# Optimization experiments

Measured on AMD Instinct MI355X. Metric: run time of the kernel, lower is better.

The kernel has to match this reference:

```python
import jax, jax.numpy as jnp
import numpy as np

Q_NODES = 100000
S_NODES = 100000
N_EDGES = 3200000
D = 3
HIDDEN = 64
OUT_DIM = 128
STAT_DIM = 3 + 2 * D  # N_i, D_avg, D_var, Delta(D), PCA(D)


def setup_inputs() -> dict:
    key = jax.random.key(0)
    ks = jax.random.split(key, 7)
    source_pos = jax.random.normal(ks[0], (S_NODES, D), dtype=jnp.float32)
    query_pos = jax.random.normal(ks[1], (Q_NODES, D), dtype=jnp.float32)
    qi = jax.random.randint(ks[2], (N_EDGES,), 0, Q_NODES, dtype=jnp.int64)
    si = jax.random.randint(ks[3], (N_EDGES,), 0, S_NODES, dtype=jnp.int64)
    edge_index = jnp.stack([qi, si], axis=0)
    # MLP params (torch Linear default-ish scale)
    W1 = jax.random.normal(ks[4], (HIDDEN, STAT_DIM), dtype=jnp.float32) / np.sqrt(STAT_DIM)
    b1 = jnp.zeros((HIDDEN,), dtype=jnp.float32)
    W2 = jax.random.normal(ks[5], (OUT_DIM, HIDDEN), dtype=jnp.float32) / np.sqrt(HIDDEN)
    b2 = jnp.zeros((OUT_DIM,), dtype=jnp.float32)
    return {"source_pos": source_pos, "query_pos": query_pos, "edge_index": edge_index,
            "W1": W1, "b1": b1, "W2": W2, "b2": b2}


def _stat_features(source_pos, query_pos, edge_index):
    Q = query_pos.shape[0]
    qi = edge_index[0]
    si = edge_index[1]
    ones = jnp.ones(qi.shape, dtype=jnp.float32)
    counts = jax.ops.segment_sum(ones, qi, num_segments=Q)          # [Q] = N_i
    has = counts > 0
    Nc = jnp.where(has, counts, 1.0)                                 # clamp 0 -> 1

    nbr = source_pos[si]                                             # [E,D]
    qc = query_pos[qi]                                               # [E,D]
    dist = jnp.linalg.norm(nbr - qc, axis=1)                         # [E]
    D_avg = jax.ops.segment_sum(dist, qi, num_segments=Q) / Nc       # [Q]
    E_X2 = jax.ops.segment_sum(dist * dist, qi, num_segments=Q) / Nc
    D_var = jnp.maximum(E_X2 - D_avg * D_avg, 0.0)

    centroid = jax.ops.segment_sum(nbr, qi, num_segments=Q) / Nc[:, None]  # [Q,D]
    Delta = centroid - query_pos                                     # [Q,D]

    centered = nbr - centroid[qi]                                    # [E,D]
    cov_comp = centered[:, :, None] * centered[:, None, :]           # [E,D,D]
    cov = jax.ops.segment_sum(cov_comp, qi, num_segments=Q) / Nc[:, None, None]

    eig = jnp.linalg.eigvalsh(cov)[:, ::-1]                          # descending [Q,D]
    PCA = jnp.where(has[:, None], eig, 0.0)

    feats = jnp.concatenate([counts[:, None], D_avg[:, None], D_var[:, None], Delta, PCA], axis=1)
    feats = jnp.where(has[:, None], feats, 0.0)

    mean = feats.mean(axis=0, keepdims=True)
    std = jnp.std(feats, axis=0, ddof=1, keepdims=True)              # torch std is unbiased
    std = jnp.where(std < 1e-6, 1.0, std)
    return (feats - mean) / std


def reference(source_pos, query_pos, edge_index, W1, b1, W2, b2):
    feats = _stat_features(source_pos, query_pos, edge_index)        # [Q, 9]
    h = jax.nn.relu(feats @ W1.T + b1)
    return h @ W2.T + b2                                             # [Q, OUT_DIM]
```

## Files before the change

kernel.cpp:

```cpp
#include <hip/hip_runtime.h>
#include <math.h>

#define Q_NODES 100000
#define S_NODES 100000
#define N_EDGES 3200000
#define HIDDEN 64
#define OUT_DIM 128

#define QPB   128
#define NB    782
#define CAPB  4608
#define TILE  8192
#define NT4   (N_EDGES / 4)

#define F_CURSOR_OFF 0
#define F_NORM_OFF   3200
#define F_PSUM_OFF   3328
#define F_PSUMSQ_OFF 31488
#define F_FEATS_OFF  59648
#define F_SP4_OFF    3659648
#define F_SLOTS_OFF  5259648
#define F_ZERO_BYTES 3200
#define F_WS_NEED    (5259648ull + (unsigned long long)(NB * CAPB + 1) * 4)

#define B_ACC_OFF    0
#define B_STATS_OFF  4800000
#define B_NORM_OFF   4800144
#define B_FEATS_OFF  4800224
#define B_ZERO_BYTES 4800144

__device__ __forceinline__ void atomAddF(float* p, float v) {
#if defined(__gfx950__) || defined(__gfx942__) || defined(__gfx90a__)
    unsafeAtomicAdd(p, v);
#else
    atomicAdd(p, v);
#endif
}


__device__ __forceinline__ void eig3_sym(
        float a00, float a01, float a02, float a11, float a12, float a22,
        float& e1, float& e2, float& e3) {
    float p1 = a01 * a01 + a02 * a02 + a12 * a12;
    float qm = (a00 + a11 + a22) * (1.0f / 3.0f);
    float b00 = a00 - qm, b11 = a11 - qm, b22 = a22 - qm;
    float p2 = b00 * b00 + b11 * b11 + b22 * b22 + 2.0f * p1;
    if (p2 <= 1e-24f) {
        e1 = qm; e2 = qm; e3 = qm;
    } else {
        float p = sqrtf(p2 * (1.0f / 6.0f));
        float invp = 1.0f / p;
        float c00 = b00 * invp, c11 = b11 * invp, c22 = b22 * invp;
        float c01 = a01 * invp, c02 = a02 * invp, c12 = a12 * invp;
        float detB = c00 * (c11 * c22 - c12 * c12)
                   - c01 * (c01 * c22 - c12 * c02)
                   + c02 * (c01 * c12 - c11 * c02);
        float r = 0.5f * detB;
        r = fminf(fmaxf(r, -1.0f), 1.0f);
        float phi = acosf(r) * (1.0f / 3.0f);
        e1 = qm + 2.0f * p * cosf(phi);
        e3 = qm + 2.0f * p * cosf(phi + 2.0943951023931953f);
        e2 = 3.0f * qm - e1 - e3;
    }
}

__device__ __forceinline__ void sums_to_feats(
        const float* s, float qx, float qy, float qz, float* f) {
    float n = s[0];
#pragma unroll
    for (int k = 0; k < 9; ++k) f[k] = 0.0f;
    if (n > 0.0f) {
        float inv = 1.0f / n;
        float Davg = s[1] * inv;
        float Dvar = fmaxf(s[2] * inv - Davg * Davg, 0.0f);
        float cx = s[3] * inv, cy = s[4] * inv, cz = s[5] * inv;
        float a00 = fmaxf(s[6] * inv - cx * cx, 0.0f);
        float a01 = s[7] * inv - cx * cy;
        float a02 = s[8] * inv - cx * cz;
        float a11 = fmaxf(s[9] * inv - cy * cy, 0.0f);
        float a12 = s[10] * inv - cy * cz;
        float a22 = fmaxf(s[11] * inv - cz * cz, 0.0f);
        float e1, e2, e3;
        eig3_sym(a00, a01, a02, a11, a12, a22, e1, e2, e3);
        f[0] = n; f[1] = Davg; f[2] = Dvar;
        f[3] = cx - qx; f[4] = cy - qy; f[5] = cz - qz;
        f[6] = e1; f[7] = e2; f[8] = e3;
    }
}


__global__ __launch_bounds__(512, 4) void partition_kernel(
        const int* __restrict__ edge,
        const float* __restrict__ sp,
        float4* __restrict__ sp4,
        int* __restrict__ cursor,
        unsigned int* __restrict__ slots) {
    __shared__ unsigned int s_rec[TILE];
    __shared__ int s_posh[TILE];
    __shared__ int s_cur[NB];
    __shared__ int s_off[NB];
    __shared__ int s_wsum[8];

    int tid = threadIdx.x;
    int lane = tid & 63, wv = tid >> 6;
    int tileStart = blockIdx.x * TILE;
    int tileCount = N_EDGES - tileStart;
    if (tileCount > TILE) tileCount = TILE;

    {
        int i = blockIdx.x * 512 + tid;
        if (i < S_NODES)
            sp4[i] = make_float4(sp[3 * i], sp[3 * i + 1], sp[3 * i + 2], 0.0f);
    }

    for (int b = tid; b < NB; b += 512) s_posh[b] = 0;
    __syncthreads();

    const int4* eq4 = (const int4*)edge;
    const int4* es4 = (const int4*)(edge + N_EDGES);
    int base4 = blockIdx.x * (TILE / 4);
    int4 q4[4], s4[4];
    bool v[4];
#pragma unroll
    for (int j = 0; j < 4; ++j) {
        int i4 = base4 + tid + j * 512;
        v[j] = i4 < NT4;
        int ic = v[j] ? i4 : 0;
        q4[j] = eq4[ic];
        s4[j] = es4[ic];
        if (v[j]) {
            atomicAdd(&s_posh[q4[j].x >> 7], 1);
            atomicAdd(&s_posh[q4[j].y >> 7], 1);
            atomicAdd(&s_posh[q4[j].z >> 7], 1);
            atomicAdd(&s_posh[q4[j].w >> 7], 1);
        }
    }
    __syncthreads();

    int local[2], tsum = 0;
#pragma unroll
    for (int j = 0; j < 2; ++j) {
        int idx = 2 * tid + j;
        local[j] = (idx < NB) ? s_posh[idx] : 0;
        tsum += local[j];
    }
    int inc = tsum;
#pragma unroll
    for (int off = 1; off < 64; off <<= 1) {
        int t = __shfl_up(inc, off);
        if (lane >= off) inc += t;
    }
    if (lane == 63) s_wsum[wv] = inc;
    __syncthreads();
    int wbase = 0;
    for (int w = 0; w < wv; ++w) wbase += s_wsum[w];
    int run = wbase + inc - tsum;
#pragma unroll
    for (int j = 0; j < 2; ++j) {
        int idx = 2 * tid + j;
        if (idx < NB) s_cur[idx] = run;
        run += local[j];
    }
    __syncthreads();

    for (int b = tid; b < NB; b += 512) {
        int c = s_posh[b];
        int base = c ? atomicAdd(&cursor[b], c) : 0;
        s_off[b] = b * CAPB + base - s_cur[b];
    }
    __syncthreads();

#pragma unroll
    for (int j = 0; j < 4; ++j) {
        if (v[j]) {
            int qs[4] = { q4[j].x, q4[j].y, q4[j].z, q4[j].w };
            int ss[4] = { s4[j].x, s4[j].y, s4[j].z, s4[j].w };
#pragma unroll
            for (int m = 0; m < 4; ++m) {
                int bkt = qs[m] >> 7;
                int idx = atomicAdd(&s_cur[bkt], 1);
                int gpos = idx + s_off[bkt];
                if (gpos >= (bkt + 1) * CAPB) gpos = NB * CAPB;
                s_rec[idx] = ((unsigned)(qs[m] & (QPB - 1)) << 17) | (unsigned)ss[m];
                s_posh[idx] = gpos;
            }
        }
    }
    __syncthreads();

    for (int i = tid; i < tileCount; i += 512)
        slots[s_posh[i]] = s_rec[i];
}

__global__ __launch_bounds__(512) void bucket_kernel(
        const int* __restrict__ cursor,
        const unsigned int* __restrict__ slots,
        const float4* __restrict__ sp4,
        const float* __restrict__ qp,
        float* __restrict__ feats,
        float* __restrict__ psum,
        float* __restrict__ psumsq) {
    __shared__ unsigned int s_sorted[CAPB];
    __shared__ float qtile[QPB * 3];
    __shared__ int s_cnt[QPB], s_start[QPB], s_cur[QPB];
    __shared__ float s_part[4][QPB][13];
    __shared__ float s_red1[8][9], s_red2[8][9];

    int tid = threadIdx.x;
    int b = blockIdx.x;
    int cnt = cursor[b];
    if (cnt > CAPB) cnt = CAPB;

    if (tid < QPB) s_cnt[tid] = 0;
    for (int i = tid; i < QPB * 3; i += 512) {
        int g = b * QPB * 3 + i;
        qtile[i] = (g < Q_NODES * 3) ? qp[g] : 0.0f;
    }
    __syncthreads();

    const unsigned int* bslots = slots + b * CAPB;
    for (int i = tid; i < cnt; i += 512)
        atomicAdd(&s_cnt[bslots[i] >> 17], 1);
    __syncthreads();

    if (tid < 64) {
        int a0 = s_cnt[tid], a1 = s_cnt[64 + tid];
        int i0 = a0, i1 = a1;
#pragma unroll
        for (int off = 1; off < 64; off <<= 1) {
            int t0 = __shfl_up(i0, off); if (tid >= off) i0 += t0;
            int t1 = __shfl_up(i1, off); if (tid >= off) i1 += t1;
        }
        int tot0 = __shfl(i0, 63);
        s_start[tid] = i0 - a0;              s_cur[tid] = i0 - a0;
        s_start[64 + tid] = i1 - a1 + tot0;  s_cur[64 + tid] = i1 - a1 + tot0;
    }
    __syncthreads();

    for (int i = tid; i < cnt; i += 512) {
        unsigned rec = bslots[i];
        int pos = atomicAdd(&s_cur[rec >> 17], 1);
        s_sorted[pos] = rec;
    }
    __syncthreads();

    {
        int q = tid & (QPB - 1);
        int sub = tid >> 7;
        float qx = qtile[3 * q + 0], qy = qtile[3 * q + 1], qz = qtile[3 * q + 2];
        float s[12];
#pragma unroll
        for (int k = 0; k < 12; ++k) s[k] = 0.0f;
        int st = s_start[q], deg = s_cnt[q];
        for (int j = sub; j < deg; j += 4) {
            unsigned rec = s_sorted[st + j];
            float4 sv = sp4[rec & 0x1FFFF];
            float dx = sv.x - qx, dy = sv.y - qy, dz = sv.z - qz;
            float d2 = dx * dx + dy * dy + dz * dz;
            s[0] += 1.0f;
            s[1] += sqrtf(d2);
            s[2] += d2;
            s[3] += sv.x; s[4] += sv.y; s[5] += sv.z;
            s[6] += sv.x * sv.x; s[7] += sv.x * sv.y; s[8] += sv.x * sv.z;
            s[9] += sv.y * sv.y; s[10] += sv.y * sv.z; s[11] += sv.z * sv.z;
        }
#pragma unroll
        for (int k = 0; k < 12; ++k) s_part[sub][q][k] = s[k];
    }
    __syncthreads();

    float f[9];
#pragma unroll
    for (int k = 0; k < 9; ++k) f[k] = 0.0f;
    int q = b * QPB + (tid & (QPB - 1));
    if (tid < QPB && q < Q_NODES) {
        float qx = qtile[3 * tid + 0], qy = qtile[3 * tid + 1], qz = qtile[3 * tid + 2];
        float s[12];
#pragma unroll
        for (int k = 0; k < 12; ++k)
            s[k] = ((s_part[0][tid][k] + s_part[1][tid][k])
                  + (s_part[2][tid][k] + s_part[3][tid][k]));
        sums_to_feats(s, qx, qy, qz, f);
#pragma unroll
        for (int k = 0; k < 9; ++k) feats[k * Q_NODES + q] = f[k];
    }

    int lane = tid & 63, wv = tid >> 6;
#pragma unroll
    for (int k = 0; k < 9; ++k) {
        float s1 = f[k];
        float s2 = f[k] * f[k];
#pragma unroll
        for (int off = 32; off > 0; off >>= 1) {
            s1 += __shfl_down(s1, off);
            s2 += __shfl_down(s2, off);
        }
        if (lane == 0) { s_red1[wv][k] = s1; s_red2[wv][k] = s2; }
    }
    __syncthreads();
    if (tid < 9) {
        float t1 = 0.0f, t2 = 0.0f;
#pragma unroll
        for (int w = 0; w < 8; ++w) { t1 += s_red1[w][tid]; t2 += s_red2[w][tid]; }
        psum[tid * NB + b]   = t1;
        psumsq[tid * NB + b] = t2;
    }
}

__global__ __launch_bounds__(576) void stats_reduce_kernel(
        const float* __restrict__ psum,
        const float* __restrict__ psumsq,
        float* __restrict__ norm) {
    int k = threadIdx.x >> 6, lane = threadIdx.x & 63;
    if (k >= 9) return;
    double a1 = 0.0, a2 = 0.0;
    for (int b = lane; b < NB; b += 64) {
        a1 += (double)psum[k * NB + b];
        a2 += (double)psumsq[k * NB + b];
    }
#pragma unroll
    for (int off = 32; off > 0; off >>= 1) {
        a1 += __shfl_down(a1, off);
        a2 += __shfl_down(a2, off);
    }
    if (lane == 0) {
        double S = a1, S2 = a2;
        double mean = S / (double)Q_NODES;
        double var = (S2 - S * S / (double)Q_NODES) / (double)(Q_NODES - 1);
        if (var < 0.0) var = 0.0;
        double sd = sqrt(var);
        if (sd < 1e-6) sd = 1.0;
        norm[k] = (float)mean;
        norm[9 + k] = (float)(1.0 / sd);
    }
}


__global__ __launch_bounds__(512, 6) void mlp_kernel(
        const float* __restrict__ feats,
        const float* __restrict__ norm,
        const float* __restrict__ W1, const float* __restrict__ b1,
        const float* __restrict__ W2, const float* __restrict__ b2,
        float* __restrict__ out) {
    __shared__ float sW1[576];
    __shared__ float sB1[64];
    __shared__ float sB2[128];
    __shared__ float sNorm[18];
    __shared__ float w2t[64 * 64];
    __shared__ float ht[64 * 128];

    int tid = threadIdx.x;
    int blk_q = blockIdx.x;

    for (int i = tid; i < 576; i += 512) sW1[i] = W1[i];
    if (tid < 64) sB1[tid] = b1[tid];
    if (tid < 128) sB2[tid] = b2[tid];
    if (tid < 18) sNorm[tid] = norm[tid];

    {
        int o = tid & 63, kc = (tid >> 6) * 8;
#pragma unroll
        for (int j = 0; j < 8; ++j) {
            int k = kc + j;
            w2t[k * 64 + o] = W2[o * 64 + k];
        }
    }
    __syncthreads();

    {
        int q = tid & 127, quarter = tid >> 7;
        int qg = blk_q * 128 + q;
        int qc = qg < Q_NODES ? qg : Q_NODES - 1;
        float f[9];
#pragma unroll
        for (int k = 0; k < 9; ++k)
            f[k] = (feats[k * Q_NODES + qc] - sNorm[k]) * sNorm[9 + k];
#pragma unroll 4
        for (int j = 0; j < 16; ++j) {
            int ko = quarter * 16 + j;
            float a = sB1[ko];
#pragma unroll
            for (int kf = 0; kf < 9; ++kf) a = fmaf(f[kf], sW1[ko * 9 + kf], a);
            ht[ko * 128 + q] = fmaxf(a, 0.0f);
        }
    }
    __syncthreads();

    int qt = tid >> 4, ot = tid & 15;
    int q0 = qt * 4, o0 = ot * 4;

#pragma unroll 1
    for (int pass = 0; pass < 2; ++pass) {
        int oh = pass * 64;
        if (pass) {
            __syncthreads();
            int o = tid & 63, kc = (tid >> 6) * 8;
#pragma unroll
            for (int j = 0; j < 8; ++j) {
                int k = kc + j;
                w2t[k * 64 + o] = W2[(oh + o) * 64 + k];
            }
            __syncthreads();
        }

        float acc[4][4];
#pragma unroll
        for (int i = 0; i < 4; ++i)
#pragma unroll
            for (int j = 0; j < 4; ++j) acc[i][j] = 0.0f;

#pragma unroll 4
        for (int k = 0; k < 64; ++k) {
            float4 h = *(const float4*)&ht[k * 128 + q0];
            float4 w = *(const float4*)&w2t[k * 64 + o0];
            float hh[4] = { h.x, h.y, h.z, h.w };
#pragma unroll
            for (int i = 0; i < 4; ++i) {
                acc[i][0] = fmaf(hh[i], w.x, acc[i][0]);
                acc[i][1] = fmaf(hh[i], w.y, acc[i][1]);
                acc[i][2] = fmaf(hh[i], w.z, acc[i][2]);
                acc[i][3] = fmaf(hh[i], w.w, acc[i][3]);
            }
        }

        float4 bb = *(const float4*)&sB2[oh + o0];
#pragma unroll
        for (int i = 0; i < 4; ++i) {
            int qg = blk_q * 128 + q0 + i;
            if (qg < Q_NODES) {
                float4 vv = make_float4(acc[i][0] + bb.x, acc[i][1] + bb.y,
                                        acc[i][2] + bb.z, acc[i][3] + bb.w);
                *(float4*)(out + (size_t)qg * 128 + oh + o0) = vv;
            }
        }
    }
}


__global__ __launch_bounds__(256) void edge_kernel(
        const int* __restrict__ edge,
        const float* __restrict__ sp,
        const float* __restrict__ qp,
        float* __restrict__ acc) {
    int e = blockIdx.x * 256 + threadIdx.x;
    if (e >= N_EDGES) return;
    int q = edge[e];
    int s = edge[N_EDGES + e];
    float sx = sp[3 * s + 0], sy = sp[3 * s + 1], sz = sp[3 * s + 2];
    float qx = qp[3 * q + 0], qy = qp[3 * q + 1], qz = qp[3 * q + 2];
    float dx = sx - qx, dy = sy - qy, dz = sz - qz;
    float d2 = dx * dx + dy * dy + dz * dz;
    atomAddF(acc + 0 * Q_NODES + q, 1.0f);
    atomAddF(acc + 1 * Q_NODES + q, sqrtf(d2));
    atomAddF(acc + 2 * Q_NODES + q, d2);
    atomAddF(acc + 3 * Q_NODES + q, sx);
    atomAddF(acc + 4 * Q_NODES + q, sy);
    atomAddF(acc + 5 * Q_NODES + q, sz);
    atomAddF(acc + 6 * Q_NODES + q, sx * sx);
    atomAddF(acc + 7 * Q_NODES + q, sx * sy);
    atomAddF(acc + 8 * Q_NODES + q, sx * sz);
    atomAddF(acc + 9 * Q_NODES + q, sy * sy);
    atomAddF(acc + 10 * Q_NODES + q, sy * sz);
    atomAddF(acc + 11 * Q_NODES + q, sz * sz);
}

__global__ __launch_bounds__(256) void finalize_kernel(
        const float* __restrict__ acc,
        const float* __restrict__ qp,
        float* __restrict__ feats,
        double* __restrict__ stats) {
    int q = blockIdx.x * 256 + threadIdx.x;
    float f[9];
#pragma unroll
    for (int k = 0; k < 9; ++k) f[k] = 0.0f;
    if (q < Q_NODES) {
        float s[12];
#pragma unroll
        for (int k = 0; k < 12; ++k) s[k] = acc[k * Q_NODES + q];
        float qx = qp[3 * q + 0], qy = qp[3 * q + 1], qz = qp[3 * q + 2];
        sums_to_feats(s, qx, qy, qz, f);
#pragma unroll
        for (int k = 0; k < 9; ++k) feats[k * Q_NODES + q] = f[k];
    }
    int lane = threadIdx.x & 63;
#pragma unroll
    for (int k = 0; k < 9; ++k) {
        float s1 = f[k];
        float s2 = f[k] * f[k];
#pragma unroll
        for (int off = 32; off > 0; off >>= 1) {
            s1 += __shfl_down(s1, off);
            s2 += __shfl_down(s2, off);
        }
        if (lane == 0) {
            atomicAdd(&stats[k], (double)s1);
            atomicAdd(&stats[9 + k], (double)s2);
        }
    }
}

__global__ void stats_kernel(const double* __restrict__ stats,
                             float* __restrict__ norm) {
    int k = threadIdx.x;
    if (k < 9) {
        double S = stats[k], S2 = stats[9 + k];
        double mean = S / (double)Q_NODES;
        double var = (S2 - S * S / (double)Q_NODES) / (double)(Q_NODES - 1);
        if (var < 0.0) var = 0.0;
        double sd = sqrt(var);
        if (sd < 1e-6) sd = 1.0;
        norm[k] = (float)mean;
        norm[9 + k] = (float)(1.0 / sd);
    }
}


extern "C" void kernel_launch(void* const* d_in, const int* in_sizes, int n_in,
                              void* d_out, int out_size, void* d_ws, size_t ws_size,
                              hipStream_t stream) {
    const float* sp   = (const float*)d_in[0];
    const float* qp   = (const float*)d_in[1];
    const int*   edge = (const int*)d_in[2];
    const float* W1   = (const float*)d_in[3];
    const float* b1   = (const float*)d_in[4];
    const float* W2   = (const float*)d_in[5];
    const float* b2   = (const float*)d_in[6];
    float* out = (float*)d_out;
    char* ws = (char*)d_ws;

    if (ws_size >= F_WS_NEED) {
        int*          cursor = (int*)(ws + F_CURSOR_OFF);
        float*        norm   = (float*)(ws + F_NORM_OFF);
        float*        psum   = (float*)(ws + F_PSUM_OFF);
        float*        psumsq = (float*)(ws + F_PSUMSQ_OFF);
        float*        feats  = (float*)(ws + F_FEATS_OFF);
        float4*       sp4    = (float4*)(ws + F_SP4_OFF);
        unsigned int* slots  = (unsigned int*)(ws + F_SLOTS_OFF);

        hipMemsetAsync(ws, 0, F_ZERO_BYTES, stream);
        partition_kernel<<<(N_EDGES + TILE - 1) / TILE, 512, 0, stream>>>(
            edge, sp, sp4, cursor, slots);
        bucket_kernel<<<NB, 512, 0, stream>>>(
            cursor, slots, sp4, qp, feats, psum, psumsq);
        stats_reduce_kernel<<<1, 576, 0, stream>>>(psum, psumsq, norm);
        mlp_kernel<<<NB, 512, 0, stream>>>(feats, norm, W1, b1, W2, b2, out);
    } else {
        float*  acc   = (float*)(ws + B_ACC_OFF);
        double* stats = (double*)(ws + B_STATS_OFF);
        float*  norm  = (float*)(ws + B_NORM_OFF);
        float*  feats = (float*)(ws + B_FEATS_OFF);

        hipMemsetAsync(ws, 0, B_ZERO_BYTES, stream);
        edge_kernel<<<N_EDGES / 256, 256, 0, stream>>>(edge, sp, qp, acc);
        finalize_kernel<<<(Q_NODES + 255) / 256, 256, 0, stream>>>(acc, qp, feats, stats);
        stats_kernel<<<1, 64, 0, stream>>>(stats, norm);
        mlp_kernel<<<NB, 512, 0, stream>>>(feats, norm, W1, b1, W2, b2, out);
    }
}
```

Baseline: 184.9 us.

## Restructure MLP second layer to read W2 via wave-uniform scalar loads

```diff
diff --git a/kernel.cpp b/kernel.cpp
--- a/kernel.cpp
+++ b/kernel.cpp
@@ -346,7 +346,6 @@
     __shared__ float sB1[64];
     __shared__ float sB2[128];
     __shared__ float sNorm[18];
-    __shared__ float w2t[64 * 64];
     __shared__ float ht[64 * 128];
 
     int tid = threadIdx.x;
@@ -356,15 +355,6 @@
     if (tid < 64) sB1[tid] = b1[tid];
     if (tid < 128) sB2[tid] = b2[tid];
     if (tid < 18) sNorm[tid] = norm[tid];
-
-    {
-        int o = tid & 63, kc = (tid >> 6) * 8;
-#pragma unroll
-        for (int j = 0; j < 8; ++j) {
-            int k = kc + j;
-            w2t[k * 64 + o] = W2[o * 64 + k];
-        }
-    }
     __syncthreads();
 
     {
@@ -386,52 +376,69 @@
     }
     __syncthreads();
 
-    int qt = tid >> 4, ot = tid & 15;
-    int q0 = qt * 4, o0 = ot * 4;
-
-#pragma unroll 1
-    for (int pass = 0; pass < 2; ++pass) {
-        int oh = pass * 64;
-        if (pass) {
-            __syncthreads();
-            int o = tid & 63, kc = (tid >> 6) * 8;
-#pragma unroll
-            for (int j = 0; j < 8; ++j) {
-                int k = kc + j;
-                w2t[k * 64 + o] = W2[(oh + o) * 64 + k];
-            }
-            __syncthreads();
-        }
-
-        float acc[4][4];
-#pragma unroll
-        for (int i = 0; i < 4; ++i)
-#pragma unroll
-            for (int j = 0; j < 4; ++j) acc[i][j] = 0.0f;
-
-#pragma unroll 4
-        for (int k = 0; k < 64; ++k) {
-            float4 h = *(const float4*)&ht[k * 128 + q0];
-            float4 w = *(const float4*)&w2t[k * 64 + o0];
-            float hh[4] = { h.x, h.y, h.z, h.w };
-#pragma unroll
-            for (int i = 0; i < 4; ++i) {
-                acc[i][0] = fmaf(hh[i], w.x, acc[i][0]);
-                acc[i][1] = fmaf(hh[i], w.y, acc[i][1]);
-                acc[i][2] = fmaf(hh[i], w.z, acc[i][2]);
-                acc[i][3] = fmaf(hh[i], w.w, acc[i][3]);
-            }
-        }
-
-        float4 bb = *(const float4*)&sB2[oh + o0];
-#pragma unroll
-        for (int i = 0; i < 4; ++i) {
-            int qg = blk_q * 128 + q0 + i;
-            if (qg < Q_NODES) {
-                float4 vv = make_float4(acc[i][0] + bb.x, acc[i][1] + bb.y,
-                                        acc[i][2] + bb.z, acc[i][3] + bb.w);
-                *(float4*)(out + (size_t)qg * 128 + oh + o0) = vv;
-            }
+    int lane = tid & 63;
+    int wvu = __builtin_amdgcn_readfirstlane(tid >> 6);
+    int o0 = wvu * 16;
+    const float4* wrow = (const float4*)(W2 + (size_t)o0 * 64);
+
+    float acc0[16], acc1[16];
+#pragma unroll
+    for (int o = 0; o < 16; ++o) { acc0[o] = 0.0f; acc1[o] = 0.0f; }
+
+    for (int kc = 0; kc < 16; ++kc) {
+        float4 w[16];
+#pragma unroll
+        for (int o = 0; o < 16; ++o) w[o] = wrow[o * 16 + kc];
+        int kb = kc * 4;
+        float h0a = ht[(kb + 0) * 128 + lane];
+        float h0b = ht[(kb + 1) * 128 + lane];
+        float h0c = ht[(kb + 2) * 128 + lane];
+        float h0d = ht[(kb + 3) * 128 + lane];
+        float h1a = ht[(kb + 0) * 128 + 64 + lane];
+        float h1b = ht[(kb + 1) * 128 + 64 + lane];
+        float h1c = ht[(kb + 2) * 128 + 64 + lane];
+        float h1d = ht[(kb + 3) * 128 + 64 + lane];
+#pragma unroll
+        for (int o = 0; o < 16; ++o) {
+            acc0[o] = fmaf(h0a, w[o].x, acc0[o]);
+            acc1[o] = fmaf(h1a, w[o].x, acc1[o]);
+            acc0[o] = fmaf(h0b, w[o].y, acc0[o]);
+            acc1[o] = fmaf(h1b, w[o].y, acc1[o]);
+            acc0[o] = fmaf(h0c, w[o].z, acc0[o]);
+            acc1[o] = fmaf(h1c, w[o].z, acc1[o]);
+            acc0[o] = fmaf(h0d, w[o].w, acc0[o]);
+            acc1[o] = fmaf(h1d, w[o].w, acc1[o]);
+        }
+    }
+
+    {
+        int qg0 = blk_q * 128 + lane;
+        int qg1 = qg0 + 64;
+        float4 b0 = *(const float4*)&sB2[o0];
+        float4 b1v = *(const float4*)&sB2[o0 + 4];
+        float4 b2v = *(const float4*)&sB2[o0 + 8];
+        float4 b3 = *(const float4*)&sB2[o0 + 12];
+        if (qg0 < Q_NODES) {
+            float* op = out + (size_t)qg0 * 128 + o0;
+            *(float4*)(op + 0)  = make_float4(acc0[0] + b0.x,  acc0[1] + b0.y,
+                                              acc0[2] + b0.z,  acc0[3] + b0.w);
+            *(float4*)(op + 4)  = make_float4(acc0[4] + b1v.x, acc0[5] + b1v.y,
+                                              acc0[6] + b1v.z, acc0[7] + b1v.w);
+            *(float4*)(op + 8)  = make_float4(acc0[8] + b2v.x, acc0[9] + b2v.y,
+                                              acc0[10] + b2v.z, acc0[11] + b2v.w);
+            *(float4*)(op + 12) = make_float4(acc0[12] + b3.x, acc0[13] + b3.y,
+                                              acc0[14] + b3.z, acc0[15] + b3.w);
+        }
+        if (qg1 < Q_NODES) {
+            float* op = out + (size_t)qg1 * 128 + o0;
+            *(float4*)(op + 0)  = make_float4(acc1[0] + b0.x,  acc1[1] + b0.y,
+                                              acc1[2] + b0.z,  acc1[3] + b0.w);
+            *(float4*)(op + 4)  = make_float4(acc1[4] + b1v.x, acc1[5] + b1v.y,
+                                              acc1[6] + b1v.z, acc1[7] + b1v.w);
+            *(float4*)(op + 8)  = make_float4(acc1[8] + b2v.x, acc1[9] + b2v.y,
+                                              acc1[10] + b2v.z, acc1[11] + b2v.w);
+            *(float4*)(op + 12) = make_float4(acc1[12] + b3.x, acc1[13] + b3.y,
+                                              acc1[14] + b3.z, acc1[15] + b3.w);
         }
     }
 }
```

Result: no change. 188.1 us (+1.7%).
